# Performance work log

Measured on AMD Instinct MI355X. Metric: run time of the kernel, lower is better.

## Reference

```python
import jax, jax.numpy as jnp
import numpy as np

TOP_K = 8
SCORE_FUNC = "sigmoid"
ROUTE_NORM = True
ROUTE_SCALE = 2.5


def setup_inputs() -> dict:
    key = jax.random.key(0)
    k1, k2, k3 = jax.random.split(key, 3)
    B, S, H, E = 4, 4096, 2048, 64
    hidden_states = jax.random.normal(k1, (B, S, H), dtype=jnp.float32)
    # nn.Linear default init scale ~ 1/sqrt(H); exact distribution irrelevant for correctness
    gate_w = jax.random.normal(k2, (E, H), dtype=jnp.float32) * (1.0 / np.sqrt(H))
    expert_bias = jax.random.normal(k3, (E,), dtype=jnp.float32) * 0.1
    return {"hidden_states": hidden_states, "expert_bias": expert_bias, "gate_w": gate_w}


def reference(hidden_states, expert_bias, gate_w):
    B, S, H = hidden_states.shape
    x = hidden_states.reshape(-1, H)  # [T, H]
    logits = jnp.einsum("th,eh->te", x, gate_w)  # [T, E]
    if SCORE_FUNC == "sigmoid":
        scores = jax.nn.sigmoid(logits.astype(jnp.float32))
    else:
        scores = jax.nn.softmax(logits.astype(jnp.float32), axis=-1)
    if expert_bias is not None:
        _, selected_experts = jax.lax.top_k(scores + expert_bias[None, :], TOP_K)
        top_scores = jnp.take_along_axis(scores, selected_experts, axis=1)
    else:
        top_scores, selected_experts = jax.lax.top_k(scores, TOP_K)
    if SCORE_FUNC == "sigmoid" and ROUTE_NORM:
        denom = jnp.sum(top_scores, axis=-1, keepdims=True) + 1e-20
        top_scores = top_scores / denom
    top_scores = top_scores * ROUTE_SCALE
    return top_scores, selected_experts
```

## Files before the change

### kernel.cpp

```cpp
#include <hip/hip_runtime.h>
#include <math.h>

#define T_TOTAL 16384
#define HDIM    2048
#define NEXP    64
#define KS_MAIN 8

typedef unsigned short ushort_t;
using bf16x8 = __attribute__((ext_vector_type(8))) short;
using f32x4  = __attribute__((ext_vector_type(4))) float;

__device__ __forceinline__ unsigned bf16rne(float f) {
    const unsigned u = __float_as_uint(f);
    return (u + 0x7FFFu + ((u >> 16) & 1u)) >> 16;
}
__device__ __forceinline__ float bf16tof(unsigned b) {
    return __uint_as_float(b << 16);
}

__device__ __forceinline__ unsigned cvtpk_bf16(float a, float b) {
    unsigned r;
    asm("v_cvt_pk_bf16_f32 %0, %1, %2" : "=v"(r) : "v"(a), "v"(b));
    return r;
}

__device__ __forceinline__ void split8(const float4 a, const float4 b,
                                       bf16x8& h, bf16x8& m, bf16x8& l) {
    const float f[8] = {a.x, a.y, a.z, a.w, b.x, b.y, b.z, b.w};
    union { unsigned u[4]; bf16x8 v; } H, M, L;
#pragma unroll
    for (int d = 0; d < 4; ++d) {
        const float f0 = f[2*d], f1 = f[2*d+1];
        const unsigned ph = cvtpk_bf16(f0, f1);
        const float r0 = f0 - __uint_as_float(ph << 16);
        const float r1 = f1 - __uint_as_float(ph & 0xFFFF0000u);
        const unsigned pm = cvtpk_bf16(r0, r1);
        const float s0 = r0 - __uint_as_float(pm << 16);
        const float s1 = r1 - __uint_as_float(pm & 0xFFFF0000u);
        H.u[d] = ph;
        M.u[d] = pm;
        L.u[d] = cvtpk_bf16(s0, s1);
    }
    h = H.v; m = M.v; l = L.v;
}

__global__ void convert_w_kernel(const float* __restrict__ w,
                                 ushort_t* __restrict__ whi,
                                 ushort_t* __restrict__ wmid,
                                 ushort_t* __restrict__ wlo)
{
    const int i = (blockIdx.x * 256 + threadIdx.x) * 4;
    const float4 v = *(const float4*)(w + i);
    float f[4] = {v.x, v.y, v.z, v.w};
#pragma unroll
    for (int j = 0; j < 4; ++j) {
        const float    x  = f[j];
        const unsigned hu = bf16rne(x);
        const float    r1 = x - bf16tof(hu);
        const unsigned mu = bf16rne(r1);
        const float    r2 = r1 - bf16tof(mu);
        const unsigned lu = bf16rne(r2);
        whi [i + j] = (ushort_t)hu;
        wmid[i + j] = (ushort_t)mu;
        wlo [i + j] = (ushort_t)lu;
    }
}

__global__ __launch_bounds__(256, 4)
void router_gemm_mfma(const float*   __restrict__ x,
                      const ushort_t* __restrict__ whi,
                      const ushort_t* __restrict__ wmid,
                      const ushort_t* __restrict__ wlo,
                      float* __restrict__ partial)
{
    constexpr int KSLICE = HDIM / KS_MAIN;
    const int tid  = threadIdx.x;
    const int wv   = tid >> 6;
    const int lane = tid & 63;
    const int tb   = blockIdx.x >> 3;
    const int ks   = blockIdx.x & 7;
    const int t0   = tb * 128 + wv * 32;
    const int k0   = ks * KSLICE;
    const int lr   = lane & 15;
    const int lg   = lane >> 4;
    const int kl   = lg * 8;

    f32x4 acc[2][4];
#pragma unroll
    for (int mt = 0; mt < 2; ++mt)
#pragma unroll
        for (int nt = 0; nt < 4; ++nt) {
            f32x4 z = {0.0f, 0.0f, 0.0f, 0.0f};
            acc[mt][nt] = z;
        }

    const float* px0 = x + (size_t)(t0 + lr) * HDIM + k0 + kl;
    const float* px1 = px0 + (size_t)16 * HDIM;

    const size_t boff = (size_t)lr * HDIM + k0 + kl;
    const ushort_t* pbh = whi  + boff;
    const ushort_t* pbm = wmid + boff;
    const ushort_t* pbl = wlo  + boff;

    float4 c00 = *(const float4*)(px0);
    float4 c01 = *(const float4*)(px0 + 4);
    float4 c10 = *(const float4*)(px1);
    float4 c11 = *(const float4*)(px1 + 4);

    bf16x8 Bh_c = *(const bf16x8*)(pbh);
    bf16x8 Bm_c = *(const bf16x8*)(pbm);
    bf16x8 Bl_c = *(const bf16x8*)(pbl);

#pragma unroll 1
    for (int kk = 0; kk < KSLICE; kk += 32) {
        bf16x8 Ah[2], Am[2], Al[2];
        split8(c00, c01, Ah[0], Am[0], Al[0]);
        split8(c10, c11, Ah[1], Am[1], Al[1]);

        if (kk + 32 < KSLICE) {
            c00 = *(const float4*)(px0 + kk + 32);
            c01 = *(const float4*)(px0 + kk + 36);
            c10 = *(const float4*)(px1 + kk + 32);
            c11 = *(const float4*)(px1 + kk + 36);
        }

#pragma unroll
        for (int nt = 0; nt < 4; ++nt) {
            const int ntn = (nt + 1) & 3;
            int kkn = (nt == 3) ? kk + 32 : kk;
            if (kkn >= KSLICE) kkn = 0;
            const size_t non = (size_t)ntn * 16 * HDIM + kkn;
            bf16x8 Bh_n = *(const bf16x8*)(pbh + non);
            bf16x8 Bm_n = *(const bf16x8*)(pbm + non);
            bf16x8 Bl_n = *(const bf16x8*)(pbl + non);

#pragma unroll
            for (int mt = 0; mt < 2; ++mt) {
                acc[mt][nt] = __builtin_amdgcn_mfma_f32_16x16x32_bf16(Ah[mt], Bh_c, acc[mt][nt], 0, 0, 0);
                acc[mt][nt] = __builtin_amdgcn_mfma_f32_16x16x32_bf16(Am[mt], Bh_c, acc[mt][nt], 0, 0, 0);
                acc[mt][nt] = __builtin_amdgcn_mfma_f32_16x16x32_bf16(Al[mt], Bh_c, acc[mt][nt], 0, 0, 0);
                acc[mt][nt] = __builtin_amdgcn_mfma_f32_16x16x32_bf16(Ah[mt], Bm_c, acc[mt][nt], 0, 0, 0);
                acc[mt][nt] = __builtin_amdgcn_mfma_f32_16x16x32_bf16(Am[mt], Bm_c, acc[mt][nt], 0, 0, 0);
                acc[mt][nt] = __builtin_amdgcn_mfma_f32_16x16x32_bf16(Ah[mt], Bl_c, acc[mt][nt], 0, 0, 0);
            }

            Bh_c = Bh_n; Bm_c = Bm_n; Bl_c = Bl_n;
        }
    }

#pragma unroll
    for (int mt = 0; mt < 2; ++mt) {
        const int trow = t0 + mt * 16 + lg * 4;
#pragma unroll
        for (int nt = 0; nt < 4; ++nt) {
            float* pb = partial + ((size_t)trow * KS_MAIN + ks) * NEXP + nt * 16 + lr;
#pragma unroll
            for (int r = 0; r < 4; ++r)
                pb[(size_t)r * KS_MAIN * NEXP] = acc[mt][nt][r];
        }
    }
}

__global__ void router_gemm_naive(const float* __restrict__ x,
                                  const float* __restrict__ w,
                                  float* __restrict__ partial)
{
    const int t = blockIdx.x;
    const int e = threadIdx.x;
    const float* xp = x + (size_t)t * HDIM;
    const float* wp = w + (size_t)e * HDIM;
    float s = 0.0f;
    for (int k = 0; k < HDIM; ++k) s = fmaf(xp[k], wp[k], s);
    partial[(size_t)t * NEXP + e] = s;
}

template<int KS>
__global__ __launch_bounds__(256)
void router_topk_kernel(const float* __restrict__ partial,
                        const float* __restrict__ bias,
                        float* __restrict__ out_scores,
                        float* __restrict__ out_idx)
{
    const int token = blockIdx.x * 4 + (threadIdx.x >> 6);
    const int lane  = threadIdx.x & 63;

    const float* pt = partial + (size_t)token * KS * NEXP + lane;
    float logit = 0.0f;
#pragma unroll
    for (int s = 0; s < KS; ++s) logit += pt[(size_t)s * NEXP];

    const float score = 1.0f / (1.0f + expf(-logit));
    float key = score + bias[lane];

    float myscore = 0.0f;
    int   myidx   = 0;
    float denom   = 0.0f;

#pragma unroll
    for (int r = 0; r < 8; ++r) {
        float bk = key;
#pragma unroll
        for (int off = 32; off > 0; off >>= 1)
            bk = fmaxf(bk, __shfl_xor(bk, off));
        const unsigned long long msk = __ballot(key == bk);
        const int bi = __ffsll(msk) - 1;
        const float wsc = __shfl(score, bi);
        denom += wsc;
        if (lane == r)  { myscore = wsc; myidx = bi; }
        if (lane == bi) key = -__builtin_inff();
    }

    const float factor = 2.5f / (denom + 1e-20f);
    if (lane < 8) {
        out_scores[(size_t)token * 8 + lane] = myscore * factor;
        out_idx  [(size_t)token * 8 + lane] = (float)myidx;
    }
}

extern "C" void kernel_launch(void* const* d_in, const int* in_sizes, int n_in,
                              void* d_out, int out_size, void* d_ws, size_t ws_size,
                              hipStream_t stream)
{
    const float* x    = (const float*)d_in[0];
    const float* bias = (const float*)d_in[1];
    const float* w    = (const float*)d_in[2];

    float* out     = (float*)d_out;
    float* partial = (float*)d_ws;

    const size_t partialBytes = (size_t)T_TOTAL * KS_MAIN * NEXP * 4;
    const size_t wplaneElems  = (size_t)NEXP * HDIM;
    const size_t needBytes    = partialBytes + 3 * wplaneElems * sizeof(ushort_t);

    if (ws_size >= needBytes) {
        ushort_t* whi  = (ushort_t*)((char*)d_ws + partialBytes);
        ushort_t* wmid = whi  + wplaneElems;
        ushort_t* wlo  = wmid + wplaneElems;

        convert_w_kernel<<<dim3(128), dim3(256), 0, stream>>>(w, whi, wmid, wlo);
        router_gemm_mfma<<<dim3(128 * KS_MAIN), dim3(256), 0, stream>>>(
            x, whi, wmid, wlo, partial);
        router_topk_kernel<KS_MAIN><<<dim3(T_TOTAL / 4), dim3(256), 0, stream>>>(
            partial, bias, out, out + (size_t)T_TOTAL * 8);
    } else {
        router_gemm_naive<<<dim3(T_TOTAL), dim3(64), 0, stream>>>(x, w, partial);
        router_topk_kernel<1><<<dim3(T_TOTAL / 4), dim3(256), 0, stream>>>(
            partial, bias, out, out + (size_t)T_TOTAL * 8);
    }
}
```

Measured before the change: 233.8 us.

## Stage activation tiles through double-buffered LDS via async global_load_lds

Activation rows are no longer loaded from global straight into registers as strided float4s. Each wave now issues global_load_lds transfers of coalesced 8-row by 32-float tiles into a double-buffered, XOR-swizzled LDS buffer, then reads its MFMA fragments back from LDS. The aim is better-coalesced, asynchronous prefetch of x that overlaps with the MFMA work. In exchange it adds 32 KB of LDS per block, which may limit occupancy under the 4-blocks launch bound, plus a block-wide barrier every k-step.

```diff
diff --git a/kernel.cpp b/kernel.cpp
--- a/kernel.cpp
+++ b/kernel.cpp
@@ -44,6 +44,12 @@
     h = H.v; m = M.v; l = L.v;
 }
 
+__device__ __forceinline__ void load_lds16(const float* g, float* lds) {
+    __builtin_amdgcn_global_load_lds(
+        (const __attribute__((address_space(1))) unsigned int*)g,
+        (__attribute__((address_space(3))) unsigned int*)lds, 16, 0, 0);
+}
+
 __global__ void convert_w_kernel(const float* __restrict__ w,
                                  ushort_t* __restrict__ whi,
                                  ushort_t* __restrict__ wmid,
@@ -74,6 +80,8 @@
                       float* __restrict__ partial)
 {
     constexpr int KSLICE = HDIM / KS_MAIN;
+    __shared__ __align__(16) float Xs[2][128 * 32];
+
     const int tid  = threadIdx.x;
     const int wv   = tid >> 6;
     const int lane = tid & 63;
@@ -83,7 +91,10 @@
     const int k0   = ks * KSLICE;
     const int lr   = lane & 15;
     const int lg   = lane >> 4;
-    const int kl   = lg * 8;
+
+    const int r8 = lane >> 3;
+    const int cc = (lane & 7) ^ r8;
+    const float* xg = x + (size_t)(t0 + r8) * HDIM + k0 + cc * 4;
 
     f32x4 acc[2][4];
 #pragma unroll
@@ -94,34 +105,41 @@
             acc[mt][nt] = z;
         }
 
-    const float* px0 = x + (size_t)(t0 + lr) * HDIM + k0 + kl;
-    const float* px1 = px0 + (size_t)16 * HDIM;
-
-    const size_t boff = (size_t)lr * HDIM + k0 + kl;
+    const size_t boff = (size_t)lr * HDIM + k0 + lg * 8;
     const ushort_t* pbh = whi  + boff;
     const ushort_t* pbm = wmid + boff;
     const ushort_t* pbl = wlo  + boff;
 
-    float4 c00 = *(const float4*)(px0);
-    float4 c01 = *(const float4*)(px0 + 4);
-    float4 c10 = *(const float4*)(px1);
-    float4 c11 = *(const float4*)(px1 + 4);
+#pragma unroll
+    for (int p = 0; p < 4; ++p)
+        load_lds16(xg + (size_t)(p * 8) * HDIM, &Xs[0][(wv * 32 + p * 8) * 32]);
 
     bf16x8 Bh_c = *(const bf16x8*)(pbh);
     bf16x8 Bm_c = *(const bf16x8*)(pbm);
     bf16x8 Bl_c = *(const bf16x8*)(pbl);
 
+    __syncthreads();
+
+    int cur = 0;
 #pragma unroll 1
     for (int kk = 0; kk < KSLICE; kk += 32) {
+        if (kk + 32 < KSLICE) {
+            const float* xn = xg + kk + 32;
+#pragma unroll
+            for (int p = 0; p < 4; ++p)
+                load_lds16(xn + (size_t)(p * 8) * HDIM,
+                           &Xs[cur ^ 1][(wv * 32 + p * 8) * 32]);
+        }
+
         bf16x8 Ah[2], Am[2], Al[2];
-        split8(c00, c01, Ah[0], Am[0], Al[0]);
-        split8(c10, c11, Ah[1], Am[1], Al[1]);
-
-        if (kk + 32 < KSLICE) {
-            c00 = *(const float4*)(px0 + kk + 32);
-            c01 = *(const float4*)(px0 + kk + 36);
-            c10 = *(const float4*)(px1 + kk + 32);
-            c11 = *(const float4*)(px1 + kk + 36);
+#pragma unroll
+        for (int mt = 0; mt < 2; ++mt) {
+            const int row  = mt * 16 + lr;
+            const int sw   = row & 7;
+            const float* rb = &Xs[cur][(wv * 32 + row) * 32];
+            const float4 c0 = *(const float4*)(rb + (((2 * lg)     ^ sw) * 4));
+            const float4 c1 = *(const float4*)(rb + (((2 * lg + 1) ^ sw) * 4));
+            split8(c0, c1, Ah[mt], Am[mt], Al[mt]);
         }
 
 #pragma unroll
@@ -143,9 +161,11 @@
                 acc[mt][nt] = __builtin_amdgcn_mfma_f32_16x16x32_bf16(Am[mt], Bm_c, acc[mt][nt], 0, 0, 0);
                 acc[mt][nt] = __builtin_amdgcn_mfma_f32_16x16x32_bf16(Ah[mt], Bl_c, acc[mt][nt], 0, 0, 0);
             }
-
             Bh_c = Bh_n; Bm_c = Bm_n; Bl_c = Bl_n;
         }
+
+        __syncthreads();
+        cur ^= 1;
     }
 
 #pragma unroll
```

After: 229.2 us. 1.02x faster.

## Fuse router GEMM and top-k into one kernel with LDS-staged weights

Applied to the files above, without the earlier changes.

Replaces the three-kernel pipeline (weight split, split-K GEMM writing partials, top-k) with one fused kernel. Each block handles 32 tokens, and its four waves each take a quarter of K. Weights are streamed into double-buffered, swizzled LDS via global_load_lds and split into bf16 planes on the fly. Partial sums are reduced through LDS before the sigmoid/top-k. This removes the large partial-buffer round trip through global memory and two extra launches. In exchange, every block now redoes the weight bf16 splitting, and the fp32 weight tile in LDS lowers occupancy.

```diff
diff --git a/kernel.cpp b/kernel.cpp
--- a/kernel.cpp
+++ b/kernel.cpp
@@ -4,19 +4,10 @@
 #define T_TOTAL 16384
 #define HDIM    2048
 #define NEXP    64
-#define KS_MAIN 8
 
 typedef unsigned short ushort_t;
 using bf16x8 = __attribute__((ext_vector_type(8))) short;
 using f32x4  = __attribute__((ext_vector_type(4))) float;
-
-__device__ __forceinline__ unsigned bf16rne(float f) {
-    const unsigned u = __float_as_uint(f);
-    return (u + 0x7FFFu + ((u >> 16) & 1u)) >> 16;
-}
-__device__ __forceinline__ float bf16tof(unsigned b) {
-    return __uint_as_float(b << 16);
-}
 
 __device__ __forceinline__ unsigned cvtpk_bf16(float a, float b) {
     unsigned r;
@@ -44,46 +35,37 @@
     h = H.v; m = M.v; l = L.v;
 }
 
-__global__ void convert_w_kernel(const float* __restrict__ w,
-                                 ushort_t* __restrict__ whi,
-                                 ushort_t* __restrict__ wmid,
-                                 ushort_t* __restrict__ wlo)
-{
-    const int i = (blockIdx.x * 256 + threadIdx.x) * 4;
-    const float4 v = *(const float4*)(w + i);
-    float f[4] = {v.x, v.y, v.z, v.w};
-#pragma unroll
-    for (int j = 0; j < 4; ++j) {
-        const float    x  = f[j];
-        const unsigned hu = bf16rne(x);
-        const float    r1 = x - bf16tof(hu);
-        const unsigned mu = bf16rne(r1);
-        const float    r2 = r1 - bf16tof(mu);
-        const unsigned lu = bf16rne(r2);
-        whi [i + j] = (ushort_t)hu;
-        wmid[i + j] = (ushort_t)mu;
-        wlo [i + j] = (ushort_t)lu;
-    }
+__device__ __forceinline__ void load_lds16(const float* g, float* lds) {
+    __builtin_amdgcn_global_load_lds(
+        (const __attribute__((address_space(1))) unsigned int*)g,
+        (__attribute__((address_space(3))) unsigned int*)lds, 16, 0, 0);
 }
 
-__global__ __launch_bounds__(256, 4)
-void router_gemm_mfma(const float*   __restrict__ x,
-                      const ushort_t* __restrict__ whi,
-                      const ushort_t* __restrict__ wmid,
-                      const ushort_t* __restrict__ wlo,
-                      float* __restrict__ partial)
+__global__ __launch_bounds__(256, 2)
+void router_fused(const float* __restrict__ x,
+                  const float* __restrict__ w,
+                  const float* __restrict__ bias,
+                  float* __restrict__ out_scores,
+                  float* __restrict__ out_idx)
 {
-    constexpr int KSLICE = HDIM / KS_MAIN;
+    __shared__ __align__(16) float S[4 * 4096];
+
     const int tid  = threadIdx.x;
     const int wv   = tid >> 6;
     const int lane = tid & 63;
-    const int tb   = blockIdx.x >> 3;
-    const int ks   = blockIdx.x & 7;
-    const int t0   = tb * 128 + wv * 32;
-    const int k0   = ks * KSLICE;
+    const int t0   = blockIdx.x * 32;
+    const int k0   = wv * 512;
     const int lr   = lane & 15;
     const int lg   = lane >> 4;
-    const int kl   = lg * 8;
+
+    float* Wbase = S + wv * 4096;
+
+    const int wrow = lane >> 3;
+    const int wchk = (lane & 7) ^ wrow;
+    const float* wg = w + (size_t)wrow * HDIM + k0 + wchk * 4;
+
+    const float* px0 = x + (size_t)(t0 + lr) * HDIM + k0 + lg * 8;
+    const float* px1 = px0 + (size_t)16 * HDIM;
 
     f32x4 acc[2][4];
 #pragma unroll
@@ -94,126 +76,103 @@
             acc[mt][nt] = z;
         }
 
-    const float* px0 = x + (size_t)(t0 + lr) * HDIM + k0 + kl;
-    const float* px1 = px0 + (size_t)16 * HDIM;
-
-    const size_t boff = (size_t)lr * HDIM + k0 + kl;
-    const ushort_t* pbh = whi  + boff;
-    const ushort_t* pbm = wmid + boff;
-    const ushort_t* pbl = wlo  + boff;
+#pragma unroll
+    for (int p = 0; p < 8; ++p)
+        load_lds16(wg + (size_t)(p * 8) * HDIM, Wbase + p * 256);
 
     float4 c00 = *(const float4*)(px0);
     float4 c01 = *(const float4*)(px0 + 4);
     float4 c10 = *(const float4*)(px1);
     float4 c11 = *(const float4*)(px1 + 4);
 
-    bf16x8 Bh_c = *(const bf16x8*)(pbh);
-    bf16x8 Bm_c = *(const bf16x8*)(pbm);
-    bf16x8 Bl_c = *(const bf16x8*)(pbl);
-
 #pragma unroll 1
-    for (int kk = 0; kk < KSLICE; kk += 32) {
+    for (int kk = 0; kk < 16; ++kk) {
         bf16x8 Ah[2], Am[2], Al[2];
         split8(c00, c01, Ah[0], Am[0], Al[0]);
         split8(c10, c11, Ah[1], Am[1], Al[1]);
 
-        if (kk + 32 < KSLICE) {
-            c00 = *(const float4*)(px0 + kk + 32);
-            c01 = *(const float4*)(px0 + kk + 36);
-            c10 = *(const float4*)(px1 + kk + 32);
-            c11 = *(const float4*)(px1 + kk + 36);
-        }
+        const int kn = ((kk + 1) & 15) * 32;
 
+        c00 = *(const float4*)(px0 + kn);
+        c01 = *(const float4*)(px0 + kn + 4);
+        c10 = *(const float4*)(px1 + kn);
+        c11 = *(const float4*)(px1 + kn + 4);
+
+        float* wd = Wbase + ((kk + 1) & 1) * 2048;
+#pragma unroll
+        for (int p = 0; p < 8; ++p)
+            load_lds16(wg + (size_t)(p * 8) * HDIM + kn, wd + p * 256);
+
+        asm volatile("s_waitcnt vmcnt(12)" ::: "memory");
+
+        const float* Wc = Wbase + (kk & 1) * 2048;
 #pragma unroll
         for (int nt = 0; nt < 4; ++nt) {
-            const int ntn = (nt + 1) & 3;
-            int kkn = (nt == 3) ? kk + 32 : kk;
-            if (kkn >= KSLICE) kkn = 0;
-            const size_t non = (size_t)ntn * 16 * HDIM + kkn;
-            bf16x8 Bh_n = *(const bf16x8*)(pbh + non);
-            bf16x8 Bm_n = *(const bf16x8*)(pbm + non);
-            bf16x8 Bl_n = *(const bf16x8*)(pbl + non);
-
+            const int e  = nt * 16 + lr;
+            const int sw = lr & 7;
+            const float* rb = Wc + e * 32;
+            const float4 b0 = *(const float4*)(rb + (((2 * lg)     ^ sw) * 4));
+            const float4 b1 = *(const float4*)(rb + (((2 * lg + 1) ^ sw) * 4));
+            bf16x8 Bh, Bm, Bl;
+            split8(b0, b1, Bh, Bm, Bl);
 #pragma unroll
             for (int mt = 0; mt < 2; ++mt) {
-                acc[mt][nt] = __builtin_amdgcn_mfma_f32_16x16x32_bf16(Ah[mt], Bh_c, acc[mt][nt], 0, 0, 0);
-                acc[mt][nt] = __builtin_amdgcn_mfma_f32_16x16x32_bf16(Am[mt], Bh_c, acc[mt][nt], 0, 0, 0);
-                acc[mt][nt] = __builtin_amdgcn_mfma_f32_16x16x32_bf16(Al[mt], Bh_c, acc[mt][nt], 0, 0, 0);
-                acc[mt][nt] = __builtin_amdgcn_mfma_f32_16x16x32_bf16(Ah[mt], Bm_c, acc[mt][nt], 0, 0, 0);
-                acc[mt][nt] = __builtin_amdgcn_mfma_f32_16x16x32_bf16(Am[mt], Bm_c, acc[mt][nt], 0, 0, 0);
-                acc[mt][nt] = __builtin_amdgcn_mfma_f32_16x16x32_bf16(Ah[mt], Bl_c, acc[mt][nt], 0, 0, 0);
+                acc[mt][nt] = __builtin_amdgcn_mfma_f32_16x16x32_bf16(Ah[mt], Bh, acc[mt][nt], 0, 0, 0);
+                acc[mt][nt] = __builtin_amdgcn_mfma_f32_16x16x32_bf16(Am[mt], Bh, acc[mt][nt], 0, 0, 0);
+                acc[mt][nt] = __builtin_amdgcn_mfma_f32_16x16x32_bf16(Al[mt], Bh, acc[mt][nt], 0, 0, 0);
+                acc[mt][nt] = __builtin_amdgcn_mfma_f32_16x16x32_bf16(Ah[mt], Bm, acc[mt][nt], 0, 0, 0);
+                acc[mt][nt] = __builtin_amdgcn_mfma_f32_16x16x32_bf16(Am[mt], Bm, acc[mt][nt], 0, 0, 0);
+                acc[mt][nt] = __builtin_amdgcn_mfma_f32_16x16x32_bf16(Ah[mt], Bl, acc[mt][nt], 0, 0, 0);
             }
-
-            Bh_c = Bh_n; Bm_c = Bm_n; Bl_c = Bl_n;
         }
     }
 
+    const float bv = bias[lane];
+
+    asm volatile("s_waitcnt vmcnt(0)" ::: "memory");
+
 #pragma unroll
-    for (int mt = 0; mt < 2; ++mt) {
-        const int trow = t0 + mt * 16 + lg * 4;
+    for (int mt = 0; mt < 2; ++mt)
 #pragma unroll
-        for (int nt = 0; nt < 4; ++nt) {
-            float* pb = partial + ((size_t)trow * KS_MAIN + ks) * NEXP + nt * 16 + lr;
+        for (int nt = 0; nt < 4; ++nt)
 #pragma unroll
             for (int r = 0; r < 4; ++r)
-                pb[(size_t)r * KS_MAIN * NEXP] = acc[mt][nt][r];
-        }
-    }
-}
+                S[wv * 4096 + (mt * 16 + lg * 4 + r) * 64 + nt * 16 + lr] = acc[mt][nt][r];
 
-__global__ void router_gemm_naive(const float* __restrict__ x,
-                                  const float* __restrict__ w,
-                                  float* __restrict__ partial)
-{
-    const int t = blockIdx.x;
-    const int e = threadIdx.x;
-    const float* xp = x + (size_t)t * HDIM;
-    const float* wp = w + (size_t)e * HDIM;
-    float s = 0.0f;
-    for (int k = 0; k < HDIM; ++k) s = fmaf(xp[k], wp[k], s);
-    partial[(size_t)t * NEXP + e] = s;
-}
+    __syncthreads();
 
-template<int KS>
-__global__ __launch_bounds__(256)
-void router_topk_kernel(const float* __restrict__ partial,
-                        const float* __restrict__ bias,
-                        float* __restrict__ out_scores,
-                        float* __restrict__ out_idx)
-{
-    const int token = blockIdx.x * 4 + (threadIdx.x >> 6);
-    const int lane  = threadIdx.x & 63;
+#pragma unroll 1
+    for (int i = 0; i < 8; ++i) {
+        const int t = wv * 8 + i;
+        const int o = t * 64 + lane;
+        const float logit = S[o] + S[4096 + o] + S[8192 + o] + S[12288 + o];
 
-    const float* pt = partial + (size_t)token * KS * NEXP + lane;
-    float logit = 0.0f;
-#pragma unroll
-    for (int s = 0; s < KS; ++s) logit += pt[(size_t)s * NEXP];
+        const float score = 1.0f / (1.0f + expf(-logit));
+        float key = score + bv;
 
-    const float score = 1.0f / (1.0f + expf(-logit));
-    float key = score + bias[lane];
-
-    float myscore = 0.0f;
-    int   myidx   = 0;
-    float denom   = 0.0f;
+        float myscore = 0.0f;
+        int   myidx   = 0;
+        float denom   = 0.0f;
 
 #pragma unroll
-    for (int r = 0; r < 8; ++r) {
-        float bk = key;
+        for (int r = 0; r < 8; ++r) {
+            float bk = key;
 #pragma unroll
-        for (int off = 32; off > 0; off >>= 1)
-            bk = fmaxf(bk, __shfl_xor(bk, off));
-        const unsigned long long msk = __ballot(key == bk);
-        const int bi = __ffsll(msk) - 1;
-        const float wsc = __shfl(score, bi);
-        denom += wsc;
-        if (lane == r)  { myscore = wsc; myidx = bi; }
-        if (lane == bi) key = -__builtin_inff();
-    }
+            for (int off = 32; off > 0; off >>= 1)
+                bk = fmaxf(bk, __shfl_xor(bk, off));
+            const unsigned long long msk = __ballot(key == bk);
+            const int bi = __ffsll((long long)msk) - 1;
+            const float wsc = __shfl(score, bi);
+            denom += wsc;
+            if (lane == r)  { myscore = wsc; myidx = bi; }
+            if (lane == bi) key = -__builtin_inff();
+        }
 
-    const float factor = 2.5f / (denom + 1e-20f);
-    if (lane < 8) {
-        out_scores[(size_t)token * 8 + lane] = myscore * factor;
-        out_idx  [(size_t)token * 8 + lane] = (float)myidx;
+        const float factor = 2.5f / (denom + 1e-20f);
+        if (lane < 8) {
+            out_scores[(size_t)(t0 + t) * 8 + lane] = myscore * factor;
+            out_idx  [(size_t)(t0 + t) * 8 + lane] = (float)myidx;
+        }
     }
 }
 
@@ -225,26 +184,8 @@
     const float* bias = (const float*)d_in[1];
     const float* w    = (const float*)d_in[2];
 
-    float* out     = (float*)d_out;
-    float* partial = (float*)d_ws;
+    float* out = (float*)d_out;
 
-    const size_t partialBytes = (size_t)T_TOTAL * KS_MAIN * NEXP * 4;
-    const size_t wplaneElems  = (size_t)NEXP * HDIM;
-    const size_t needBytes    = partialBytes + 3 * wplaneElems * sizeof(ushort_t);
-
-    if (ws_size >= needBytes) {
-        ushort_t* whi  = (ushort_t*)((char*)d_ws + partialBytes);
-        ushort_t* wmid = whi  + wplaneElems;
-        ushort_t* wlo  = wmid + wplaneElems;
-
-        convert_w_kernel<<<dim3(128), dim3(256), 0, stream>>>(w, whi, wmid, wlo);
-        router_gemm_mfma<<<dim3(128 * KS_MAIN), dim3(256), 0, stream>>>(
-            x, whi, wmid, wlo, partial);
-        router_topk_kernel<KS_MAIN><<<dim3(T_TOTAL / 4), dim3(256), 0, stream>>>(
-            partial, bias, out, out + (size_t)T_TOTAL * 8);
-    } else {
-        router_gemm_naive<<<dim3(T_TOTAL), dim3(64), 0, stream>>>(x, w, partial);
-        router_topk_kernel<1><<<dim3(T_TOTAL / 4), dim3(256), 0, stream>>>(
-            partial, bias, out, out + (size_t)T_TOTAL * 8);
-    }
+    router_fused<<<dim3(T_TOTAL / 32), dim3(256), 0, stream>>>(
+        x, w, bias, out, out + (size_t)T_TOTAL * 8);
 }
```

Measured after the change: 217.0 us. 1.08x faster.
